# Kernel tuning notes

Hardware: AMD Instinct MI355X
Metric: run time of the kernel (lower is better)

The kernel has to match this reference:

```python
import jax, jax.numpy as jnp
import numpy as np


def setup_inputs() -> dict:
    key = jax.random.key(0)
    k1, k2, k3 = jax.random.split(key, 3)
    B, Tq, Tv, D = 4, 4096, 4096, 64
    return {
        "query": jax.random.normal(k1, (B, Tq, D), dtype=jnp.float32),
        "value": jax.random.normal(k2, (B, Tv, D), dtype=jnp.float32),
        "key": jax.random.normal(k3, (B, Tv, D), dtype=jnp.float32),
        "q_mask": jnp.ones((B, Tq), dtype=bool),
        "v_mask": jnp.ones((B, Tv), dtype=bool),
        "scale": jnp.ones((1,), dtype=jnp.float32),  # tied trainable scale, init 'one'
    }


def reference(query, value, key, q_mask, v_mask, scale):
    # scores: [B, Tq, Tv] = (scale * Q) @ K^T  (attention_type='mul')
    scores = jnp.einsum("bqd,bkd->bqk", scale * query, key)
    Tq, Tv = scores.shape[1], scores.shape[2]
    # causal lower-triangular mask [1, Tq, Tv] AND value mask [B, 1, Tv]
    causal = jnp.tril(jnp.ones((Tq, Tv), dtype=bool))[None, :, :]
    scores_mask = jnp.logical_and(v_mask[:, None, :], causal)
    # additive -1e9 masking, then softmax over Tv
    scores = scores - 1e9 * (~scores_mask).astype(scores.dtype)
    attn = jax.nn.softmax(scores, axis=-1)
    # weighted sum: [B, Tq, dim]
    out = jnp.einsum("bqk,bkd->bqd", attn, value)
    # zero out masked query positions
    out = out * q_mask[:, :, None].astype(out.dtype)
    return out
```

## Files before the change

### kernel.cpp

```cpp
#include <hip/hip_runtime.h>


#define B_SZ   4
#define T_SEQ  4096
#define D_HEAD 64
#define NW     8
#define PSTR   72
#define THR    10.0f

typedef _Float16 half4v __attribute__((ext_vector_type(4)));
typedef _Float16 half8v __attribute__((ext_vector_type(8)));
typedef float    f32x4  __attribute__((ext_vector_type(4)));

__device__ __forceinline__ float fexp2(float x) {
#if __has_builtin(__builtin_amdgcn_exp2f)
    return __builtin_amdgcn_exp2f(x);
#else
    return exp2f(x);
#endif
}

template <int CTRL>
__device__ __forceinline__ float dppf(float x) {
    return __builtin_bit_cast(float,
        __builtin_amdgcn_update_dpp(0, __builtin_bit_cast(int, x), CTRL, 0xF, 0xF, false));
}
__device__ __forceinline__ float rowmax16(float x) {
    x = fmaxf(x, dppf<0xB1>(x));
    x = fmaxf(x, dppf<0x4E>(x));
    x = fmaxf(x, dppf<0x141>(x));
    x = fmaxf(x, dppf<0x140>(x));
    return x;
}
__device__ __forceinline__ float rowsum16(float x) {
    x += dppf<0xB1>(x);
    x += dppf<0x4E>(x);
    x += dppf<0x141>(x);
    x += dppf<0x140>(x);
    return x;
}

__global__ __launch_bounds__(256) void prep_kv(const float* __restrict__ K,
                                               const float* __restrict__ V,
                                               _Float16* __restrict__ Ks,
                                               _Float16* __restrict__ Vs) {
    const int bid = blockIdx.x;
    const int tid = threadIdx.x;
    if (bid < 1024) {
        const int u   = bid * 256 + tid;
        const int d4  = (u & 15) * 4;
        const int kg  = u >> 4;
        const int b   = kg >> 12;
        const int key = kg & 4095;
        const int k16 = key >> 4, kc = key & 15;
        const float4 f = *reinterpret_cast<const float4*>(K + (size_t)kg * D_HEAD + d4);
        half4v hv = {(_Float16)f.x, (_Float16)f.y, (_Float16)f.z, (_Float16)f.w};
        const int h = d4 >> 5, quad = (d4 & 31) >> 3, j0 = d4 & 7;
        *reinterpret_cast<half4v*>(
            Ks + (((size_t)b * 256 + k16) * 2 + h) * 512 + (quad * 16 + kc) * 8 + j0) = hv;
    } else {
        const int u    = (bid - 1024) * 256 + tid;
        const int jh   = u & 1;
        const int l    = (u >> 1) & 63;
        const int nb   = (u >> 7) & 3;
        const int g32  = (u >> 9) & 127;
        const int b    = u >> 16;
        const int quad = l >> 4, cc = l & 15;
        const float* vb = V + ((size_t)b * T_SEQ + g32 * 32 + quad * 8 + jh * 4) * D_HEAD
                            + nb * 16 + cc;
        half4v hv;
#pragma unroll
        for (int j = 0; j < 4; ++j) hv[j] = (_Float16)vb[(size_t)j * D_HEAD];
        *reinterpret_cast<half4v*>(
            Vs + (((size_t)b * 128 + g32) * 4 + nb) * 512 + l * 8 + jh * 4) = hv;
    }
}

__global__ __launch_bounds__(512, 4) void attn_fwd(
    const float* __restrict__ Q, const _Float16* __restrict__ Ks,
    const _Float16* __restrict__ Vs, const float* __restrict__ scale_p,
    float* __restrict__ Out)
{
    const int tid  = threadIdx.x;
    const int lane = tid & 63;
    const int wave = tid >> 6;
    const int c    = lane & 15;
    const int quad = lane >> 4;

    const int b     = blockIdx.x & 3;
    const int tile  = 255 - (blockIdx.x >> 2);
    const int qbase = tile << 4;
    const float scale = scale_p[0] * 1.44269504089f;

    __shared__ __align__(16) char smem[NW * 16 * 64 * 4];
    _Float16* wp = reinterpret_cast<_Float16*>(smem) + wave * (16 * PSTR);
    float* o_sh  = reinterpret_cast<float*>(smem);
    __shared__ float m_sh[NW][16], l_sh[NW][16];

    const float* qrow = Q + ((size_t)b * T_SEQ + qbase + c) * D_HEAD;
    half8v aq[2];
#pragma unroll
    for (int h = 0; h < 2; ++h) {
        const float4 f0 = *reinterpret_cast<const float4*>(qrow + h * 32 + quad * 8);
        const float4 f1 = *reinterpret_cast<const float4*>(qrow + h * 32 + quad * 8 + 4);
        aq[h][0] = (_Float16)(f0.x * scale); aq[h][1] = (_Float16)(f0.y * scale);
        aq[h][2] = (_Float16)(f0.z * scale); aq[h][3] = (_Float16)(f0.w * scale);
        aq[h][4] = (_Float16)(f1.x * scale); aq[h][5] = (_Float16)(f1.y * scale);
        aq[h][6] = (_Float16)(f1.z * scale); aq[h][7] = (_Float16)(f1.w * scale);
    }

    f32x4 o[4];
#pragma unroll
    for (int nb = 0; nb < 4; ++nb) o[nb] = (f32x4){0.f, 0.f, 0.f, 0.f};
    float m_r[4] = {-1e30f, -1e30f, -1e30f, -1e30f};
    float l_r[4] = {0.f, 0.f, 0.f, 0.f};

    const int kmax = qbase + 15;
    const _Float16* Ksb = Ks + (size_t)b * (T_SEQ / 16) * 2 * 512;
    const _Float16* Vsb = Vs + (size_t)b * (T_SEQ / 32) * 4 * 512;

    auto kstep = [&](int j0, bool masked) {
        const _Float16* kp = Ksb + (size_t)(j0 >> 4) * 2 * 512 + lane * 8;
        half8v kf[4][2];
#pragma unroll
        for (int kb = 0; kb < 4; ++kb)
#pragma unroll
            for (int h = 0; h < 2; ++h)
                kf[kb][h] = *reinterpret_cast<const half8v*>(kp + (kb * 2 + h) * 512);

        f32x4 s[4];
#pragma unroll
        for (int kb = 0; kb < 4; ++kb) s[kb] = (f32x4){0.f, 0.f, 0.f, 0.f};
#pragma unroll
        for (int h = 0; h < 2; ++h)
#pragma unroll
            for (int kb = 0; kb < 4; ++kb)
                s[kb] = __builtin_amdgcn_mfma_f32_16x16x32_f16(aq[h], kf[kb][h], s[kb], 0, 0, 0);

        const _Float16* vp = Vsb + (size_t)(j0 >> 5) * 4 * 512 + lane * 8;
        half8v vf[2][4];
#pragma unroll
        for (int kh = 0; kh < 2; ++kh)
#pragma unroll
            for (int nb = 0; nb < 4; ++nb)
                vf[kh][nb] = *reinterpret_cast<const half8v*>(vp + kh * 2048 + nb * 512);

        if (masked) {
#pragma unroll
            for (int r = 0; r < 4; ++r) {
                const int row = qbase + quad * 4 + r;
#pragma unroll
                for (int kb = 0; kb < 4; ++kb)
                    s[kb][r] = (j0 + kb * 16 + c <= row) ? s[kb][r] : -1e30f;
            }
        }

        float tmax[4];
#pragma unroll
        for (int r = 0; r < 4; ++r)
            tmax[r] = fmaxf(fmaxf(s[0][r], s[1][r]), fmaxf(s[2][r], s[3][r]));

        float e[4][4];
        bool near = true;
#pragma unroll
        for (int r = 0; r < 4; ++r) near = near && (tmax[r] <= m_r[r] + THR);

        if (!masked && __all(near)) {
#pragma unroll
            for (int r = 0; r < 4; ++r) {
#pragma unroll
                for (int kb = 0; kb < 4; ++kb) e[kb][r] = fexp2(s[kb][r] - m_r[r]);
                l_r[r] += (e[0][r] + e[1][r]) + (e[2][r] + e[3][r]);
            }
        } else {
            float alpha[4];
#pragma unroll
            for (int r = 0; r < 4; ++r) {
                const float mx = rowmax16(tmax[r]);
                const float mn = fmaxf(m_r[r], mx);
                const float al = fexp2(m_r[r] - mn);
#pragma unroll
                for (int kb = 0; kb < 4; ++kb) e[kb][r] = fexp2(s[kb][r] - mn);
                l_r[r] = l_r[r] * al + ((e[0][r] + e[1][r]) + (e[2][r] + e[3][r]));
                m_r[r] = mn;
                alpha[r] = al;
            }
#pragma unroll
            for (int nb = 0; nb < 4; ++nb)
#pragma unroll
                for (int r = 0; r < 4; ++r) o[nb][r] *= alpha[r];
        }

#pragma unroll
        for (int r = 0; r < 4; ++r)
#pragma unroll
            for (int kb = 0; kb < 4; ++kb)
                wp[(quad * 4 + r) * PSTR + kb * 16 + c] = (_Float16)e[kb][r];

        const half8v pf0 = *reinterpret_cast<const half8v*>(wp + c * PSTR + quad * 8);
        const half8v pf1 = *reinterpret_cast<const half8v*>(wp + c * PSTR + 32 + quad * 8);

#pragma unroll
        for (int nb = 0; nb < 4; ++nb)
            o[nb] = __builtin_amdgcn_mfma_f32_16x16x32_f16(pf0, vf[0][nb], o[nb], 0, 0, 0);
#pragma unroll
        for (int nb = 0; nb < 4; ++nb)
            o[nb] = __builtin_amdgcn_mfma_f32_16x16x32_f16(pf1, vf[1][nb], o[nb], 0, 0, 0);
    };

    for (int j0 = wave * 64; j0 + 64 <= qbase; j0 += NW * 64)
        kstep(j0, false);

    const int j_tail = kmax & ~63;
    if (wave == ((j_tail >> 6) & (NW - 1)))
        kstep(j_tail, true);

    float lrow[4];
#pragma unroll
    for (int r = 0; r < 4; ++r) lrow[r] = rowsum16(l_r[r]);

    __syncthreads();

#pragma unroll
    for (int r = 0; r < 4; ++r) {
        const int rl = quad * 4 + r;
#pragma unroll
        for (int nb = 0; nb < 4; ++nb) o_sh[(wave * 16 + rl) * 64 + nb * 16 + c] = o[nb][r];
        if (c == 0) { m_sh[wave][rl] = m_r[r]; l_sh[wave][rl] = lrow[r]; }
    }
    __syncthreads();

    const int row = tid >> 5;
    const int d   = (tid & 31) * 2;
    float mstar = m_sh[0][row];
#pragma unroll
    for (int w = 1; w < NW; ++w) mstar = fmaxf(mstar, m_sh[w][row]);
    float lsum = 0.f, a0 = 0.f, a1 = 0.f;
#pragma unroll
    for (int w = 0; w < NW; ++w) {
        const float mw = m_sh[w][row];
        const float wgt = (mw > -1e29f) ? fexp2(mw - mstar) : 0.f;
        lsum += wgt * l_sh[w][row];
        a0 += wgt * o_sh[(w * 16 + row) * 64 + d];
        a1 += wgt * o_sh[(w * 16 + row) * 64 + d + 1];
    }
    const float inv = (lsum > 0.f) ? 1.0f / lsum : 0.f;
    float* op = Out + ((size_t)b * T_SEQ + qbase + row) * D_HEAD + d;
    float2 st = {a0 * inv, a1 * inv};
    *reinterpret_cast<float2*>(op) = st;
}

extern "C" void kernel_launch(void* const* d_in, const int* in_sizes, int n_in,
                              void* d_out, int out_size, void* d_ws, size_t ws_size,
                              hipStream_t stream) {
    const float* Q = (const float*)d_in[0];
    const float* V = (const float*)d_in[1];
    const float* K = (const float*)d_in[2];
    const float* sc = (const float*)d_in[5];
    float* out = (float*)d_out;

    const size_t N = (size_t)B_SZ * T_SEQ * D_HEAD;
    _Float16* Ks = (_Float16*)d_ws;
    _Float16* Vs = Ks + N;

    prep_kv<<<dim3(2048), dim3(256), 0, stream>>>(K, V, Ks, Vs);
    attn_fwd<<<dim3(B_SZ * 256), dim3(512), 0, stream>>>(Q, Ks, Vs, sc, out);
}
```

Baseline: 110.8 us.

## Process 32 query rows per block with 32-key steps to reuse K/V fragments

```diff
diff --git a/kernel.cpp b/kernel.cpp
--- a/kernel.cpp
+++ b/kernel.cpp
@@ -5,7 +5,7 @@
 #define T_SEQ  4096
 #define D_HEAD 64
 #define NW     8
-#define PSTR   72
+#define PSTR   40
 #define THR    10.0f
 
 typedef _Float16 half4v __attribute__((ext_vector_type(4)));
@@ -76,7 +76,7 @@
     }
 }
 
-__global__ __launch_bounds__(512, 4) void attn_fwd(
+__global__ __launch_bounds__(512, 2) void attn_fwd(
     const float* __restrict__ Q, const _Float16* __restrict__ Ks,
     const _Float16* __restrict__ Vs, const float* __restrict__ scale_p,
     float* __restrict__ Out)
@@ -88,166 +88,191 @@
     const int quad = lane >> 4;
 
     const int b     = blockIdx.x & 3;
-    const int tile  = 255 - (blockIdx.x >> 2);
-    const int qbase = tile << 4;
+    const int tile  = 127 - (blockIdx.x >> 2);
+    const int qbase = tile << 5;
     const float scale = scale_p[0] * 1.44269504089f;
 
-    __shared__ __align__(16) char smem[NW * 16 * 64 * 4];
-    _Float16* wp = reinterpret_cast<_Float16*>(smem) + wave * (16 * PSTR);
+    __shared__ __align__(16) char smem[NW * 32 * 64 * 4];
+    _Float16* wp = reinterpret_cast<_Float16*>(smem) + wave * (2 * 16 * PSTR);
     float* o_sh  = reinterpret_cast<float*>(smem);
-    __shared__ float m_sh[NW][16], l_sh[NW][16];
-
-    const float* qrow = Q + ((size_t)b * T_SEQ + qbase + c) * D_HEAD;
-    half8v aq[2];
-#pragma unroll
-    for (int h = 0; h < 2; ++h) {
-        const float4 f0 = *reinterpret_cast<const float4*>(qrow + h * 32 + quad * 8);
-        const float4 f1 = *reinterpret_cast<const float4*>(qrow + h * 32 + quad * 8 + 4);
-        aq[h][0] = (_Float16)(f0.x * scale); aq[h][1] = (_Float16)(f0.y * scale);
-        aq[h][2] = (_Float16)(f0.z * scale); aq[h][3] = (_Float16)(f0.w * scale);
-        aq[h][4] = (_Float16)(f1.x * scale); aq[h][5] = (_Float16)(f1.y * scale);
-        aq[h][6] = (_Float16)(f1.z * scale); aq[h][7] = (_Float16)(f1.w * scale);
+    __shared__ float m_sh[NW][32], l_sh[NW][32];
+
+    half8v aq[2][2];
+#pragma unroll
+    for (int mt = 0; mt < 2; ++mt) {
+        const float* qrow = Q + ((size_t)b * T_SEQ + qbase + mt * 16 + c) * D_HEAD;
+#pragma unroll
+        for (int h = 0; h < 2; ++h) {
+            const float4 f0 = *reinterpret_cast<const float4*>(qrow + h * 32 + quad * 8);
+            const float4 f1 = *reinterpret_cast<const float4*>(qrow + h * 32 + quad * 8 + 4);
+            aq[mt][h][0] = (_Float16)(f0.x * scale); aq[mt][h][1] = (_Float16)(f0.y * scale);
+            aq[mt][h][2] = (_Float16)(f0.z * scale); aq[mt][h][3] = (_Float16)(f0.w * scale);
+            aq[mt][h][4] = (_Float16)(f1.x * scale); aq[mt][h][5] = (_Float16)(f1.y * scale);
+            aq[mt][h][6] = (_Float16)(f1.z * scale); aq[mt][h][7] = (_Float16)(f1.w * scale);
+        }
     }
 
-    f32x4 o[4];
-#pragma unroll
-    for (int nb = 0; nb < 4; ++nb) o[nb] = (f32x4){0.f, 0.f, 0.f, 0.f};
-    float m_r[4] = {-1e30f, -1e30f, -1e30f, -1e30f};
-    float l_r[4] = {0.f, 0.f, 0.f, 0.f};
-
-    const int kmax = qbase + 15;
+    f32x4 o[2][4];
+#pragma unroll
+    for (int mt = 0; mt < 2; ++mt)
+#pragma unroll
+        for (int nb = 0; nb < 4; ++nb) o[mt][nb] = (f32x4){0.f, 0.f, 0.f, 0.f};
+    float m_r[2][4], l_r[2][4];
+#pragma unroll
+    for (int mt = 0; mt < 2; ++mt)
+#pragma unroll
+        for (int r = 0; r < 4; ++r) { m_r[mt][r] = -1e30f; l_r[mt][r] = 0.f; }
+
     const _Float16* Ksb = Ks + (size_t)b * (T_SEQ / 16) * 2 * 512;
     const _Float16* Vsb = Vs + (size_t)b * (T_SEQ / 32) * 4 * 512;
 
-    auto kstep = [&](int j0, bool masked) {
+    auto body = [&](int j0, bool masked) {
         const _Float16* kp = Ksb + (size_t)(j0 >> 4) * 2 * 512 + lane * 8;
-        half8v kf[4][2];
-#pragma unroll
-        for (int kb = 0; kb < 4; ++kb)
+        half8v kf[2][2];
+#pragma unroll
+        for (int kb = 0; kb < 2; ++kb)
 #pragma unroll
             for (int h = 0; h < 2; ++h)
                 kf[kb][h] = *reinterpret_cast<const half8v*>(kp + (kb * 2 + h) * 512);
 
-        f32x4 s[4];
-#pragma unroll
-        for (int kb = 0; kb < 4; ++kb) s[kb] = (f32x4){0.f, 0.f, 0.f, 0.f};
+        const _Float16* vp = Vsb + (size_t)(j0 >> 5) * 4 * 512 + lane * 8;
+        half8v vf[4];
+#pragma unroll
+        for (int nb = 0; nb < 4; ++nb)
+            vf[nb] = *reinterpret_cast<const half8v*>(vp + nb * 512);
+
+        f32x4 s[2][2];
+#pragma unroll
+        for (int mt = 0; mt < 2; ++mt)
+#pragma unroll
+            for (int kb = 0; kb < 2; ++kb) s[mt][kb] = (f32x4){0.f, 0.f, 0.f, 0.f};
+        __builtin_amdgcn_s_setprio(1);
 #pragma unroll
         for (int h = 0; h < 2; ++h)
 #pragma unroll
-            for (int kb = 0; kb < 4; ++kb)
-                s[kb] = __builtin_amdgcn_mfma_f32_16x16x32_f16(aq[h], kf[kb][h], s[kb], 0, 0, 0);
-
-        const _Float16* vp = Vsb + (size_t)(j0 >> 5) * 4 * 512 + lane * 8;
-        half8v vf[2][4];
-#pragma unroll
-        for (int kh = 0; kh < 2; ++kh)
+            for (int mt = 0; mt < 2; ++mt) {
+                s[mt][0] = __builtin_amdgcn_mfma_f32_16x16x32_f16(aq[mt][h], kf[0][h], s[mt][0], 0, 0, 0);
+                s[mt][1] = __builtin_amdgcn_mfma_f32_16x16x32_f16(aq[mt][h], kf[1][h], s[mt][1], 0, 0, 0);
+            }
+        __builtin_amdgcn_s_setprio(0);
+
+        if (masked) {
+#pragma unroll
+            for (int mt = 0; mt < 2; ++mt)
+#pragma unroll
+                for (int r = 0; r < 4; ++r) {
+                    const int row = qbase + mt * 16 + quad * 4 + r;
+                    s[mt][0][r] = (j0 + c <= row)      ? s[mt][0][r] : -1e30f;
+                    s[mt][1][r] = (j0 + 16 + c <= row) ? s[mt][1][r] : -1e30f;
+                }
+        }
+
+        bool near = true;
+#pragma unroll
+        for (int mt = 0; mt < 2; ++mt)
+#pragma unroll
+            for (int r = 0; r < 4; ++r)
+                near = near && (fmaxf(s[mt][0][r], s[mt][1][r]) <= m_r[mt][r] + THR);
+
+        float e[2][2][4];
+        if (!masked && __all(near)) {
+#pragma unroll
+            for (int mt = 0; mt < 2; ++mt)
+#pragma unroll
+                for (int r = 0; r < 4; ++r) {
+                    e[mt][0][r] = fexp2(s[mt][0][r] - m_r[mt][r]);
+                    e[mt][1][r] = fexp2(s[mt][1][r] - m_r[mt][r]);
+                    l_r[mt][r] += e[mt][0][r] + e[mt][1][r];
+                }
+        } else {
+            float alpha[2][4];
+#pragma unroll
+            for (int mt = 0; mt < 2; ++mt)
+#pragma unroll
+                for (int r = 0; r < 4; ++r) {
+                    const float mx = rowmax16(fmaxf(s[mt][0][r], s[mt][1][r]));
+                    const float mn = fmaxf(m_r[mt][r], mx);
+                    const float al = fexp2(m_r[mt][r] - mn);
+                    e[mt][0][r] = fexp2(s[mt][0][r] - mn);
+                    e[mt][1][r] = fexp2(s[mt][1][r] - mn);
+                    l_r[mt][r] = l_r[mt][r] * al + (e[mt][0][r] + e[mt][1][r]);
+                    m_r[mt][r] = mn;
+                    alpha[mt][r] = al;
+                }
+#pragma unroll
+            for (int mt = 0; mt < 2; ++mt)
+#pragma unroll
+                for (int nb = 0; nb < 4; ++nb)
+#pragma unroll
+                    for (int r = 0; r < 4; ++r) o[mt][nb][r] *= alpha[mt][r];
+        }
+
+#pragma unroll
+        for (int mt = 0; mt < 2; ++mt)
+#pragma unroll
+            for (int r = 0; r < 4; ++r) {
+                const int row = mt * 16 + quad * 4 + r;
+                wp[row * PSTR + c]      = (_Float16)e[mt][0][r];
+                wp[row * PSTR + 16 + c] = (_Float16)e[mt][1][r];
+            }
+        const half8v pf0 = *reinterpret_cast<const half8v*>(wp + c * PSTR + quad * 8);
+        const half8v pf1 = *reinterpret_cast<const half8v*>(wp + (16 + c) * PSTR + quad * 8);
+
+        __builtin_amdgcn_s_setprio(1);
+#pragma unroll
+        for (int nb = 0; nb < 4; ++nb)
+            o[0][nb] = __builtin_amdgcn_mfma_f32_16x16x32_f16(pf0, vf[nb], o[0][nb], 0, 0, 0);
+#pragma unroll
+        for (int nb = 0; nb < 4; ++nb)
+            o[1][nb] = __builtin_amdgcn_mfma_f32_16x16x32_f16(pf1, vf[nb], o[1][nb], 0, 0, 0);
+        __builtin_amdgcn_s_setprio(0);
+    };
+
+    for (int j0 = wave * 32; j0 + 32 <= qbase; j0 += NW * 32)
+        body(j0, false);
+
+    if (wave == ((qbase >> 5) & (NW - 1)))
+        body(qbase, true);
+
+    float lrow[2][4];
+#pragma unroll
+    for (int mt = 0; mt < 2; ++mt)
+#pragma unroll
+        for (int r = 0; r < 4; ++r) lrow[mt][r] = rowsum16(l_r[mt][r]);
+
+    __syncthreads();
+
+#pragma unroll
+    for (int mt = 0; mt < 2; ++mt)
+#pragma unroll
+        for (int r = 0; r < 4; ++r) {
+            const int rl = mt * 16 + quad * 4 + r;
 #pragma unroll
             for (int nb = 0; nb < 4; ++nb)
-                vf[kh][nb] = *reinterpret_cast<const half8v*>(vp + kh * 2048 + nb * 512);
-
-        if (masked) {
-#pragma unroll
-            for (int r = 0; r < 4; ++r) {
-                const int row = qbase + quad * 4 + r;
-#pragma unroll
-                for (int kb = 0; kb < 4; ++kb)
-                    s[kb][r] = (j0 + kb * 16 + c <= row) ? s[kb][r] : -1e30f;
-            }
-        }
-
-        float tmax[4];
-#pragma unroll
-        for (int r = 0; r < 4; ++r)
-            tmax[r] = fmaxf(fmaxf(s[0][r], s[1][r]), fmaxf(s[2][r], s[3][r]));
-
-        float e[4][4];
-        bool near = true;
-#pragma unroll
-        for (int r = 0; r < 4; ++r) near = near && (tmax[r] <= m_r[r] + THR);
-
-        if (!masked && __all(near)) {
-#pragma unroll
-            for (int r = 0; r < 4; ++r) {
-#pragma unroll
-                for (int kb = 0; kb < 4; ++kb) e[kb][r] = fexp2(s[kb][r] - m_r[r]);
-                l_r[r] += (e[0][r] + e[1][r]) + (e[2][r] + e[3][r]);
-            }
-        } else {
-            float alpha[4];
-#pragma unroll
-            for (int r = 0; r < 4; ++r) {
-                const float mx = rowmax16(tmax[r]);
-                const float mn = fmaxf(m_r[r], mx);
-                const float al = fexp2(m_r[r] - mn);
-#pragma unroll
-                for (int kb = 0; kb < 4; ++kb) e[kb][r] = fexp2(s[kb][r] - mn);
-                l_r[r] = l_r[r] * al + ((e[0][r] + e[1][r]) + (e[2][r] + e[3][r]));
-                m_r[r] = mn;
-                alpha[r] = al;
-            }
-#pragma unroll
-            for (int nb = 0; nb < 4; ++nb)
-#pragma unroll
-                for (int r = 0; r < 4; ++r) o[nb][r] *= alpha[r];
-        }
-
-#pragma unroll
-        for (int r = 0; r < 4; ++r)
-#pragma unroll
-            for (int kb = 0; kb < 4; ++kb)
-                wp[(quad * 4 + r) * PSTR + kb * 16 + c] = (_Float16)e[kb][r];
-
-        const half8v pf0 = *reinterpret_cast<const half8v*>(wp + c * PSTR + quad * 8);
-        const half8v pf1 = *reinterpret_cast<const half8v*>(wp + c * PSTR + 32 + quad * 8);
-
-#pragma unroll
-        for (int nb = 0; nb < 4; ++nb)
-            o[nb] = __builtin_amdgcn_mfma_f32_16x16x32_f16(pf0, vf[0][nb], o[nb], 0, 0, 0);
-#pragma unroll
-        for (int nb = 0; nb < 4; ++nb)
-            o[nb] = __builtin_amdgcn_mfma_f32_16x16x32_f16(pf1, vf[1][nb], o[nb], 0, 0, 0);
-    };
-
-    for (int j0 = wave * 64; j0 + 64 <= qbase; j0 += NW * 64)
-        kstep(j0, false);
-
-    const int j_tail = kmax & ~63;
-    if (wave == ((j_tail >> 6) & (NW - 1)))
-        kstep(j_tail, true);
-
-    float lrow[4];
-#pragma unroll
-    for (int r = 0; r < 4; ++r) lrow[r] = rowsum16(l_r[r]);
-
+                o_sh[(wave * 32 + rl) * 64 + nb * 16 + c] = o[mt][nb][r];
+            if (c == 0) { m_sh[wave][rl] = m_r[mt][r]; l_sh[wave][rl] = lrow[mt][r]; }
+        }
     __syncthreads();
 
-#pragma unroll
-    for (int r = 0; r < 4; ++r) {
-        const int rl = quad * 4 + r;
-#pragma unroll
-        for (int nb = 0; nb < 4; ++nb) o_sh[(wave * 16 + rl) * 64 + nb * 16 + c] = o[nb][r];
-        if (c == 0) { m_sh[wave][rl] = m_r[r]; l_sh[wave][rl] = lrow[r]; }
-    }
-    __syncthreads();
-
-    const int row = tid >> 5;
-    const int d   = (tid & 31) * 2;
+    const int row = tid >> 4;
+    const int d0  = (tid & 15) * 4;
     float mstar = m_sh[0][row];
 #pragma unroll
     for (int w = 1; w < NW; ++w) mstar = fmaxf(mstar, m_sh[w][row]);
-    float lsum = 0.f, a0 = 0.f, a1 = 0.f;
+    float lsum = 0.f;
+    float a[4] = {0.f, 0.f, 0.f, 0.f};
 #pragma unroll
     for (int w = 0; w < NW; ++w) {
         const float mw = m_sh[w][row];
         const float wgt = (mw > -1e29f) ? fexp2(mw - mstar) : 0.f;
         lsum += wgt * l_sh[w][row];
-        a0 += wgt * o_sh[(w * 16 + row) * 64 + d];
-        a1 += wgt * o_sh[(w * 16 + row) * 64 + d + 1];
+        const float4 ov = *reinterpret_cast<const float4*>(&o_sh[(w * 32 + row) * 64 + d0]);
+        a[0] += wgt * ov.x; a[1] += wgt * ov.y; a[2] += wgt * ov.z; a[3] += wgt * ov.w;
     }
     const float inv = (lsum > 0.f) ? 1.0f / lsum : 0.f;
-    float* op = Out + ((size_t)b * T_SEQ + qbase + row) * D_HEAD + d;
-    float2 st = {a0 * inv, a1 * inv};
-    *reinterpret_cast<float2*>(op) = st;
+    float* op = Out + ((size_t)b * T_SEQ + qbase + row) * D_HEAD + d0;
+    float4 st = {a[0] * inv, a[1] * inv, a[2] * inv, a[3] * inv};
+    *reinterpret_cast<float4*>(op) = st;
 }
 
 extern "C" void kernel_launch(void* const* d_in, const int* in_sizes, int n_in,
@@ -264,5 +289,5 @@
     _Float16* Vs = Ks + N;
 
     prep_kv<<<dim3(2048), dim3(256), 0, stream>>>(K, V, Ks, Vs);
-    attn_fwd<<<dim3(B_SZ * 256), dim3(512), 0, stream>>>(Q, Ks, Vs, sc, out);
-}
+    attn_fwd<<<dim3(B_SZ * 128), dim3(512), 0, stream>>>(Q, Ks, Vs, sc, out);
+}
```

New measurement: 103.5 us. -6.6%, faster.
